# Kernel optimization log

Measured on AMD Instinct MI355X. Metric: run time of the kernel, lower is better.

The kernel has to match this reference:

```python
import jax, jax.numpy as jnp
import numpy as np

N_QUBITS = 10
N_LAYERS = 3
DIM = 2 ** N_QUBITS
N_ANGLES = N_LAYERS * N_QUBITS * 3


def _ring_perm(n):
    """Combined index permutation for the 'ring' CNOT sequence (q0->q1, ..., q_{n-2}->q_{n-1}, q_{n-1}->q0).
    Qubit 0 is the most significant bit, matching bin(i).zfill(n) in the original.
    Each CNOT matrix is a permutation (involution): new_state[j] = old_state[perm[j]]."""
    def cnot_perm(control, target):
        i = np.arange(2 ** n)
        ctrl = (i >> (n - 1 - control)) & 1
        return np.where(ctrl == 1, i ^ (1 << (n - 1 - target)), i)
    total = np.arange(2 ** n)
    pairs = [(q, q + 1) for q in range(n - 1)] + [(n - 1, 0)]
    for c, t in pairs:
        total = total[cnot_perm(c, t)]
    return jnp.asarray(total)

_RING = _ring_perm(N_QUBITS)


def _single_qubit_rot(angles):
    """angles: (S, n_qubits, 3) real -> (S, n_qubits, 2, 2) complex64 Rot(phi, theta, omega)."""
    phi, theta, omega = angles[..., 0], angles[..., 1], angles[..., 2]
    ct = jnp.cos(theta / 2)
    st = jnp.sin(theta / 2)
    ppo = (phi + omega) / 2
    pmo = (phi - omega) / 2
    e_m_ppo = jnp.exp(-1j * ppo)  # complex64
    e_p_ppo = jnp.exp(1j * ppo)
    e_m_pmo = jnp.exp(-1j * pmo)
    e_p_pmo = jnp.exp(1j * pmo)
    m00 = e_m_ppo * ct
    m01 = -e_p_pmo * st
    m10 = e_m_pmo * st
    m11 = e_p_ppo * ct
    S, n = angles.shape[0], angles.shape[1]
    return jnp.stack((m00, m01, m10, m11), axis=2).reshape(S, n, 2, 2)


def _system_unitary(M):
    """Batched Kronecker product over qubits: (S, n, 2, 2) -> (S, 2^n, 2^n).
    Qubit 0 is the most significant index, matching the original einsum string."""
    S = M.shape[0]
    U = M[:, 0]
    d = 2
    for q in range(1, N_QUBITS):
        U = jnp.einsum('aij,akl->aikjl', U, M[:, q]).reshape(S, d * 2, d * 2)
        d *= 2
    return U


def _forward(X, weights, bias):
    S, F = X.shape
    num_reps = N_ANGLES // F + 1
    X_exp = jnp.tile(X, (1, num_reps))[:, :N_ANGLES].reshape(S, N_LAYERS, N_QUBITS, 3)
    angles = X_exp * weights[None] + bias[None]  # (S, L, n, 3)
    state = jnp.zeros((S, DIM), dtype=jnp.complex64).at[:, 0].set(1.0)
    for l in range(N_LAYERS):
        U = _system_unitary(_single_qubit_rot(angles[:, l]))  # (S, 2^n, 2^n)
        state = jnp.einsum('bij,bj->bi', U, state)            # apply Rot layer
        state = state[:, _RING]                               # ring of CNOTs
    return state


def setup_inputs() -> dict:
    key = jax.random.key(0)
    kx, kw, kb = jax.random.split(key, 3)
    X = jax.random.uniform(kx, (32, 20), dtype=jnp.float32)
    weights = jax.random.uniform(kw, (N_LAYERS, N_QUBITS, 3), dtype=jnp.float32)
    bias = jax.random.uniform(kb, (N_LAYERS, N_QUBITS, 3), dtype=jnp.float32)
    return {"X": X, "weights": weights, "bias": bias}


def reference(X, weights, bias):
    return _forward(X, weights, bias)
```

## Files before the change

### kernel.cpp

```cpp
#include <hip/hip_runtime.h>

namespace {

constexpr int NQ   = 10;
constexpr int DIM  = 1024;
constexpr int NL   = 3;
constexpr int FEAT = 20;
constexpr int S    = 32;
constexpr int APL  = 4;

__device__ __forceinline__ float2 cmul(float2 a, float2 b) {
    return make_float2(a.x * b.x - a.y * b.y, a.x * b.y + a.y * b.x);
}
__device__ __forceinline__ float2 cmad(float2 a, float2 b, float2 acc) {
    acc.x += a.x * b.x - a.y * b.y;
    acc.y += a.x * b.y + a.y * b.x;
    return acc;
}
__device__ __forceinline__ float2 gate2(float2 ca, float2 s0, float2 cb, float2 s1) {
    float2 r;
    r.x = ca.x * s0.x - ca.y * s0.y + cb.x * s1.x - cb.y * s1.y;
    r.y = ca.x * s0.y + ca.y * s0.x + cb.x * s1.y + cb.y * s1.x;
    return r;
}

__global__ __launch_bounds__(256) void qsim(const float* __restrict__ X,
                                            const float* __restrict__ W,
                                            const float* __restrict__ Bb,
                                            float* __restrict__ out,
                                            int write_imag)
{
    const int s    = blockIdx.x;
    const int tid  = threadIdx.x;
    const int wave = tid >> 6;
    const int lane = tid & 63;

    __shared__ float2 gmat[NL * NQ][4];
    __shared__ float2 M4[NL][16];
    __shared__ float2 pbuf[DIM];

    int rlow[APL], rrow[APL];
#pragma unroll
    for (int j = 0; j < APL; ++j) {
        int r = wave * 256 + j * 64 + lane;
        if (r & 1) r ^= 1 << 9;
#pragma unroll
        for (int c = 8; c >= 0; --c)
            if ((r >> (9 - c)) & 1) r ^= 1 << (8 - c);
        rlow[j] = r & 255;
        rrow[j] = r >> 8;
    }

    if (tid < NL * NQ) {
        const int base = tid * 3;
        const float phi   = X[s * FEAT + (base    ) % FEAT] * W[base    ] + Bb[base    ];
        const float theta = X[s * FEAT + (base + 1) % FEAT] * W[base + 1] + Bb[base + 1];
        const float omega = X[s * FEAT + (base + 2) % FEAT] * W[base + 2] + Bb[base + 2];
        float sn, ct;  sincosf(0.5f * theta,         &sn, &ct);
        float sp, cp;  sincosf(0.5f * (phi + omega), &sp, &cp);
        float sm, cm;  sincosf(0.5f * (phi - omega), &sm, &cm);
        gmat[tid][0] = make_float2( cp * ct, -sp * ct);
        gmat[tid][1] = make_float2(-cm * sn, -sm * sn);
        gmat[tid][2] = make_float2( cm * sn, -sm * sn);
        gmat[tid][3] = make_float2( cp * ct,  sp * ct);
    }
    if (tid < NL * 16) {
        const int l = tid >> 4, e = tid & 15, r = e >> 2, k = e & 3;
        const float2 g0 = gmat[l * NQ + 0][(r >> 1) * 2 + (k >> 1)];
        const float2 g1 = gmat[l * NQ + 1][(r & 1) * 2 + (k & 1)];
        M4[l][e] = cmul(g0, g1);
    }
    __syncthreads();

    float2 amp[APL];
#pragma unroll
    for (int j = 0; j < APL; ++j) amp[j] = make_float2(0.f, 0.f);
    if (wave == 0 && lane == 0) amp[0] = make_float2(1.f, 0.f);

    for (int l = 0; l < NL; ++l) {
        float2 g[8][4];
#pragma unroll
        for (int q = 2; q < 10; ++q) {
#pragma unroll
            for (int e = 0; e < 4; ++e) g[q - 2][e] = gmat[l * NQ + q][e];
        }

#pragma unroll
        for (int q = 4; q < 10; ++q) {
            const int  mask = 1 << (9 - q);
            const bool hi   = (lane & mask) != 0;
            const float2 ca = hi ? g[q - 2][3] : g[q - 2][0];
            const float2 cb = hi ? g[q - 2][2] : g[q - 2][1];
            float2 o[APL];
#pragma unroll
            for (int j = 0; j < APL; ++j) {
                o[j].x = __shfl_xor(amp[j].x, mask);
                o[j].y = __shfl_xor(amp[j].y, mask);
            }
#pragma unroll
            for (int j = 0; j < APL; ++j) amp[j] = gate2(ca, amp[j], cb, o[j]);
        }

        {
            const float2 m00 = g[1][0], m01 = g[1][1], m10 = g[1][2], m11 = g[1][3];
            float2 a, c;
            a = amp[0]; c = amp[1]; amp[0] = gate2(m00, a, m01, c); amp[1] = gate2(m10, a, m11, c);
            a = amp[2]; c = amp[3]; amp[2] = gate2(m00, a, m01, c); amp[3] = gate2(m10, a, m11, c);
        }
        {
            const float2 m00 = g[0][0], m01 = g[0][1], m10 = g[0][2], m11 = g[0][3];
            float2 a, c;
            a = amp[0]; c = amp[2]; amp[0] = gate2(m00, a, m01, c); amp[2] = gate2(m10, a, m11, c);
            a = amp[1]; c = amp[3]; amp[1] = gate2(m00, a, m01, c); amp[3] = gate2(m10, a, m11, c);
        }

        if (l) __syncthreads();
#pragma unroll
        for (int j = 0; j < APL; ++j)
            pbuf[wave * 256 + j * 64 + lane] = amp[j];
        __syncthreads();
#pragma unroll
        for (int j = 0; j < APL; ++j) {
            const float2* Mrow = &M4[l][rrow[j] * 4];
            float2 acc = make_float2(0.f, 0.f);
#pragma unroll
            for (int k = 0; k < 4; ++k)
                acc = cmad(Mrow[k], pbuf[rlow[j] + (k << 8)], acc);
            amp[j] = acc;
        }
    }

    const int base_o = s * DIM + wave * 256 + lane;
#pragma unroll
    for (int j = 0; j < APL; ++j) out[base_o + j * 64] = amp[j].x;
    if (write_imag) {
#pragma unroll
        for (int j = 0; j < APL; ++j) out[S * DIM + base_o + j * 64] = amp[j].y;
    }
}

}

extern "C" void kernel_launch(void* const* d_in, const int* in_sizes, int n_in,
                              void* d_out, int out_size, void* d_ws, size_t ws_size,
                              hipStream_t stream) {
    const float* X = (const float*)d_in[0];
    const float* W = (const float*)d_in[1];
    const float* B = (const float*)d_in[2];
    (void)in_sizes; (void)n_in; (void)d_ws; (void)ws_size;
    const int write_imag = (out_size >= 2 * S * DIM) ? 1 : 0;
    qsim<<<S, 256, 0, stream>>>(X, W, B, (float*)d_out, write_imag);
}
```

Baseline: 62.14 us.

## Compute gate matrices per wave and double-buffer pbuf to drop barriers

Each wave now computes its own copy of the 30 rotation matrices and M4 products in private shared memory slices, so the initial block-wide barrier is no longer needed. The permutation buffer is double-buffered by layer parity, which removes the pre-write barrier in later layers. Gate coefficients are read from LDS inside the loop rather than being held in registers. The cost is four times the transcendental setup work, extra LDS footprint and more LDS reads per gate; correctness of the per-wave matrices depends on wave-level execution ordering without an explicit wave barrier.

```diff
diff --git a/kernel.cpp b/kernel.cpp
--- a/kernel.cpp
+++ b/kernel.cpp
@@ -8,6 +8,7 @@
 constexpr int FEAT = 20;
 constexpr int S    = 32;
 constexpr int APL  = 4;
+constexpr int NW   = 4;
 
 __device__ __forceinline__ float2 cmul(float2 a, float2 b) {
     return make_float2(a.x * b.x - a.y * b.y, a.x * b.y + a.y * b.x);
@@ -35,9 +36,29 @@
     const int wave = tid >> 6;
     const int lane = tid & 63;
 
-    __shared__ float2 gmat[NL * NQ][4];
-    __shared__ float2 M4[NL][16];
-    __shared__ float2 pbuf[DIM];
+    __shared__ float2 gm[NW][NL * NQ][4];
+    __shared__ float2 M4[NW][NL][16];
+    __shared__ float2 pbuf[2][DIM];
+
+    if (lane < NL * NQ) {
+        const int base = lane * 3;
+        const float phi   = X[s * FEAT + (base    ) % FEAT] * W[base    ] + Bb[base    ];
+        const float theta = X[s * FEAT + (base + 1) % FEAT] * W[base + 1] + Bb[base + 1];
+        const float omega = X[s * FEAT + (base + 2) % FEAT] * W[base + 2] + Bb[base + 2];
+        float sn, ct;  sincosf(0.5f * theta,         &sn, &ct);
+        float sp, cp;  sincosf(0.5f * (phi + omega), &sp, &cp);
+        float sm, cm;  sincosf(0.5f * (phi - omega), &sm, &cm);
+        gm[wave][lane][0] = make_float2( cp * ct, -sp * ct);
+        gm[wave][lane][1] = make_float2(-cm * sn, -sm * sn);
+        gm[wave][lane][2] = make_float2( cm * sn, -sm * sn);
+        gm[wave][lane][3] = make_float2( cp * ct,  sp * ct);
+    }
+    if (lane < NL * 16) {
+        const int l = lane >> 4, e = lane & 15, r = e >> 2, k = e & 3;
+        const float2 g0 = gm[wave][l * NQ + 0][(r >> 1) * 2 + (k >> 1)];
+        const float2 g1 = gm[wave][l * NQ + 1][(r & 1) * 2 + (k & 1)];
+        M4[wave][l][e] = cmul(g0, g1);
+    }
 
     int rlow[APL], rrow[APL];
 #pragma unroll
@@ -51,46 +72,18 @@
         rrow[j] = r >> 8;
     }
 
-    if (tid < NL * NQ) {
-        const int base = tid * 3;
-        const float phi   = X[s * FEAT + (base    ) % FEAT] * W[base    ] + Bb[base    ];
-        const float theta = X[s * FEAT + (base + 1) % FEAT] * W[base + 1] + Bb[base + 1];
-        const float omega = X[s * FEAT + (base + 2) % FEAT] * W[base + 2] + Bb[base + 2];
-        float sn, ct;  sincosf(0.5f * theta,         &sn, &ct);
-        float sp, cp;  sincosf(0.5f * (phi + omega), &sp, &cp);
-        float sm, cm;  sincosf(0.5f * (phi - omega), &sm, &cm);
-        gmat[tid][0] = make_float2( cp * ct, -sp * ct);
-        gmat[tid][1] = make_float2(-cm * sn, -sm * sn);
-        gmat[tid][2] = make_float2( cm * sn, -sm * sn);
-        gmat[tid][3] = make_float2( cp * ct,  sp * ct);
-    }
-    if (tid < NL * 16) {
-        const int l = tid >> 4, e = tid & 15, r = e >> 2, k = e & 3;
-        const float2 g0 = gmat[l * NQ + 0][(r >> 1) * 2 + (k >> 1)];
-        const float2 g1 = gmat[l * NQ + 1][(r & 1) * 2 + (k & 1)];
-        M4[l][e] = cmul(g0, g1);
-    }
-    __syncthreads();
-
     float2 amp[APL];
 #pragma unroll
     for (int j = 0; j < APL; ++j) amp[j] = make_float2(0.f, 0.f);
     if (wave == 0 && lane == 0) amp[0] = make_float2(1.f, 0.f);
 
     for (int l = 0; l < NL; ++l) {
-        float2 g[8][4];
-#pragma unroll
-        for (int q = 2; q < 10; ++q) {
-#pragma unroll
-            for (int e = 0; e < 4; ++e) g[q - 2][e] = gmat[l * NQ + q][e];
-        }
-
 #pragma unroll
         for (int q = 4; q < 10; ++q) {
             const int  mask = 1 << (9 - q);
-            const bool hi   = (lane & mask) != 0;
-            const float2 ca = hi ? g[q - 2][3] : g[q - 2][0];
-            const float2 cb = hi ? g[q - 2][2] : g[q - 2][1];
+            const int  hi   = (lane & mask) ? 1 : 0;
+            const float2 ca = gm[wave][l * NQ + q][hi ? 3 : 0];
+            const float2 cb = gm[wave][l * NQ + q][hi ? 2 : 1];
             float2 o[APL];
 #pragma unroll
             for (int j = 0; j < APL; ++j) {
@@ -102,30 +95,32 @@
         }
 
         {
-            const float2 m00 = g[1][0], m01 = g[1][1], m10 = g[1][2], m11 = g[1][3];
+            const float2 m00 = gm[wave][l * NQ + 3][0], m01 = gm[wave][l * NQ + 3][1];
+            const float2 m10 = gm[wave][l * NQ + 3][2], m11 = gm[wave][l * NQ + 3][3];
             float2 a, c;
             a = amp[0]; c = amp[1]; amp[0] = gate2(m00, a, m01, c); amp[1] = gate2(m10, a, m11, c);
             a = amp[2]; c = amp[3]; amp[2] = gate2(m00, a, m01, c); amp[3] = gate2(m10, a, m11, c);
         }
         {
-            const float2 m00 = g[0][0], m01 = g[0][1], m10 = g[0][2], m11 = g[0][3];
+            const float2 m00 = gm[wave][l * NQ + 2][0], m01 = gm[wave][l * NQ + 2][1];
+            const float2 m10 = gm[wave][l * NQ + 2][2], m11 = gm[wave][l * NQ + 2][3];
             float2 a, c;
             a = amp[0]; c = amp[2]; amp[0] = gate2(m00, a, m01, c); amp[2] = gate2(m10, a, m11, c);
             a = amp[1]; c = amp[3]; amp[1] = gate2(m00, a, m01, c); amp[3] = gate2(m10, a, m11, c);
         }
 
-        if (l) __syncthreads();
+        float2* buf = pbuf[l & 1];
 #pragma unroll
         for (int j = 0; j < APL; ++j)
-            pbuf[wave * 256 + j * 64 + lane] = amp[j];
+            buf[wave * 256 + j * 64 + lane] = amp[j];
         __syncthreads();
 #pragma unroll
         for (int j = 0; j < APL; ++j) {
-            const float2* Mrow = &M4[l][rrow[j] * 4];
+            const float2* Mrow = &M4[wave][l][rrow[j] * 4];
             float2 acc = make_float2(0.f, 0.f);
 #pragma unroll
             for (int k = 0; k < 4; ++k)
-                acc = cmad(Mrow[k], pbuf[rlow[j] + (k << 8)], acc);
+                acc = cmad(Mrow[k], buf[rlow[j] + (k << 8)], acc);
             amp[j] = acc;
         }
     }
```

Measured after the change: 61.24 us. No clear change (-1.5%).
